# Optimization experiments

Hardware: AMD Instinct MI355X
Metric: run time of the kernel (lower is better)

The kernel has to match this reference:

```python
import jax, jax.numpy as jnp
import numpy as np

M = 4        # num_modalities
C = 128      # in_channels
NH = 4       # num_heads
HD = C // NH # head_dim = 32
OUT = 128    # out_channels
B, D, H, W = 1, 12, 12, 12
N = D * H * W
EPS = 1e-5
SCALE = float(np.sqrt(HD))


def setup_inputs() -> dict:
    key = jax.random.key(0)
    ks = jax.random.split(key, 12)
    inp = {}
    for i in range(M):
        inp[f"feat{i}"] = jax.random.normal(ks[i], (B, C, D, H, W), dtype=jnp.float32)
    s = 1.0 / np.sqrt(C)
    inp["Wq"] = jax.random.normal(ks[4], (M, C, C), dtype=jnp.float32) * s
    inp["Wk"] = jax.random.normal(ks[5], (M, C, C), dtype=jnp.float32) * s
    inp["Wv"] = jax.random.normal(ks[6], (M, C, C), dtype=jnp.float32) * s
    inp["Wout"] = jax.random.normal(ks[7], (OUT, C), dtype=jnp.float32) * s
    inp["bn_gamma"] = jnp.ones((OUT,), jnp.float32)
    inp["bn_beta"] = jnp.zeros((OUT,), jnp.float32)
    inp["bn_mean"] = jax.random.normal(ks[8], (OUT,), dtype=jnp.float32) * 0.1
    inp["bn_var"] = jax.random.uniform(ks[9], (OUT,), dtype=jnp.float32, minval=0.5, maxval=1.5)
    return inp


def _proj(Wm, feats):
    # per-modality 1x1 conv == matmul over channels: [M,C,C] x [M,B,C,N] -> [M,B,nh,N,hd]
    p = jnp.einsum('moc,mbcn->mbon', Wm, feats)
    return p.reshape(M, B, NH, HD, N).transpose(0, 1, 2, 4, 3)


def reference(feat0, feat1, feat2, feat3, Wq, Wk, Wv, Wout,
              bn_gamma, bn_beta, bn_mean, bn_var):
    feats = jnp.stack([feat0, feat1, feat2, feat3]).reshape(M, B, C, N)
    Q = _proj(Wq, feats)   # [M,B,nh,N,hd]
    K = _proj(Wk, feats)
    V = _proj(Wv, feats)
    # concat K/V over modalities along token axis -> [B,nh,M*N,hd]
    Kall = K.transpose(1, 2, 0, 3, 4).reshape(B, NH, M * N, HD)
    Vall = V.transpose(1, 2, 0, 3, 4).reshape(B, NH, M * N, HD)
    fused = jnp.zeros((B, NH, N, HD), jnp.float32)
    for i in range(M):  # small fixed loop over modalities
        attn = jnp.einsum('bhqd,bhkd->bhqk', Q[i], Kall) / SCALE  # [B,nh,N,M*N]
        attn = jax.nn.softmax(attn, axis=-1)  # dropout is identity at eval
        fused = fused + jnp.einsum('bhqk,bhkd->bhqd', attn, Vall)
    fused = fused.transpose(0, 1, 3, 2).reshape(B, C, N)
    # out_proj: 1x1 Conv3d -> BN (eval, running stats) -> ReLU
    y = jnp.einsum('oc,bcn->bon', Wout, fused)
    inv = bn_gamma / jnp.sqrt(bn_var + EPS)
    y = y * inv[None, :, None] + (bn_beta - bn_mean * inv)[None, :, None]
    return jax.nn.relu(y).reshape(B, OUT, D, H, W)
```

## Files before the change

kernel.cpp:

```cpp
#include <hip/hip_runtime.h>

#define MODS 4
#define CH   128
#define NHD  4
#define HDIM 32
#define NTOK 1728
#define NG   (NTOK/4)
#define NKEY (MODS*NTOK)
#define NT   27
#define QSC (0.17677669529663687f * 1.4426950408889634f)

#ifndef __has_builtin
#define __has_builtin(x) 0
#endif
#if __has_builtin(__builtin_amdgcn_exp2f)
#define EXP2(x) __builtin_amdgcn_exp2f(x)
#else
#define EXP2(x) __expf(0.69314718055994531f * (x))
#endif

typedef __bf16 bf16x8 __attribute__((ext_vector_type(8)));
typedef float  f32x16 __attribute__((ext_vector_type(16)));
typedef unsigned int u32x4 __attribute__((ext_vector_type(4)));

__device__ inline bf16x8 ldb8(const unsigned short* p) {
    return *reinterpret_cast<const bf16x8*>(p);
}
__device__ inline unsigned int pkbf(float a, float b) {
    unsigned short ua = __builtin_bit_cast(unsigned short, (__bf16)a);
    unsigned short ub = __builtin_bit_cast(unsigned short, (__bf16)b);
    return (unsigned int)ua | ((unsigned int)ub << 16);
}
__device__ inline void glds16(const unsigned short* g, unsigned short* l) {
    __builtin_amdgcn_global_load_lds(
        (const __attribute__((address_space(1))) unsigned int*)(g),
        (__attribute__((address_space(3))) unsigned int*)(l), 16, 0, 0);
}

__global__ __launch_bounds__(256) void proj_kernel(
    const float* __restrict__ f0, const float* __restrict__ f1,
    const float* __restrict__ f2, const float* __restrict__ f3,
    const float* __restrict__ Wq, const float* __restrict__ Wk,
    const float* __restrict__ Wv,
    unsigned short* __restrict__ Qb, unsigned short* __restrict__ Kb,
    unsigned short* __restrict__ V2)
{
    __shared__ __align__(16) float Wt[64][68];
    __shared__ __align__(16) float fs[64][68];

    const int tid = threadIdx.x;
    const int bid = blockIdx.x;
    const int tm  = bid / 54;
    const int rem = bid % 54;
    const int oh  = rem & 1;
    const int nt  = rem >> 1;
    const int t   = tm >> 2, m = tm & 3;
    const int nb  = nt * 64;

    const float* fsrc = (m == 0) ? f0 : (m == 1) ? f1 : (m == 2) ? f2 : f3;
    const float* W    = ((t == 0) ? Wq : (t == 1) ? Wk : Wv) + (size_t)m * CH * CH;

    const int o0 = (tid >> 4) * 4, nn0 = (tid & 15) * 4;
    float acc[4][4] = {};

    for (int ch = 0; ch < 2; ++ch) {
        if (ch) __syncthreads();
        {
            const int o = tid & 63, c4b = tid >> 6;
            #pragma unroll
            for (int j = 0; j < 4; ++j) {
                const int c4 = c4b + 4 * j;
                float4 wv = *reinterpret_cast<const float4*>(
                    W + (size_t)(oh * 64 + o) * CH + ch * 64 + c4 * 4);
                Wt[c4*4+0][o] = wv.x; Wt[c4*4+1][o] = wv.y;
                Wt[c4*4+2][o] = wv.z; Wt[c4*4+3][o] = wv.w;
            }
        }
        {
            const int nchunk = tid & 15, cb = tid >> 4;
            #pragma unroll
            for (int j = 0; j < 4; ++j) {
                const int c = cb + 16 * j;
                float4 v = *reinterpret_cast<const float4*>(
                    fsrc + (size_t)(ch * 64 + c) * NTOK + nb + nchunk * 4);
                *reinterpret_cast<float4*>(&fs[c][nchunk * 4]) = v;
            }
        }
        __syncthreads();
        #pragma unroll 4
        for (int c = 0; c < 64; ++c) {
            float4 wv = *reinterpret_cast<const float4*>(&Wt[c][o0]);
            float4 fv = *reinterpret_cast<const float4*>(&fs[c][nn0]);
            acc[0][0] = fmaf(wv.x, fv.x, acc[0][0]); acc[0][1] = fmaf(wv.x, fv.y, acc[0][1]);
            acc[0][2] = fmaf(wv.x, fv.z, acc[0][2]); acc[0][3] = fmaf(wv.x, fv.w, acc[0][3]);
            acc[1][0] = fmaf(wv.y, fv.x, acc[1][0]); acc[1][1] = fmaf(wv.y, fv.y, acc[1][1]);
            acc[1][2] = fmaf(wv.y, fv.z, acc[1][2]); acc[1][3] = fmaf(wv.y, fv.w, acc[1][3]);
            acc[2][0] = fmaf(wv.z, fv.x, acc[2][0]); acc[2][1] = fmaf(wv.z, fv.y, acc[2][1]);
            acc[2][2] = fmaf(wv.z, fv.z, acc[2][2]); acc[2][3] = fmaf(wv.z, fv.w, acc[2][3]);
            acc[3][0] = fmaf(wv.w, fv.x, acc[3][0]); acc[3][1] = fmaf(wv.w, fv.y, acc[3][1]);
            acc[3][2] = fmaf(wv.w, fv.z, acc[3][2]); acc[3][3] = fmaf(wv.w, fv.w, acc[3][3]);
        }
    }

    const int og0 = oh * 64 + o0;
    const int h = og0 >> 5, d0 = og0 & 31;
    const int ng = nb + nn0;
    if (t == 2) {
        const int off = ng & 15;
        const int ng2 = (ng & ~15) + ((off & 4) << 1) + ((off & 8) >> 1);
        #pragma unroll
        for (int i = 0; i < 4; ++i) {
            ushort4 pk;
            pk.x = __builtin_bit_cast(unsigned short, (__bf16)acc[i][0]);
            pk.y = __builtin_bit_cast(unsigned short, (__bf16)acc[i][1]);
            pk.z = __builtin_bit_cast(unsigned short, (__bf16)acc[i][2]);
            pk.w = __builtin_bit_cast(unsigned short, (__bf16)acc[i][3]);
            *reinterpret_cast<ushort4*>(V2 + (size_t)(h * HDIM + d0 + i) * NKEY + m * NTOK + ng2) = pk;
        }
    } else {
        const float sc = (t == 0) ? QSC : 1.0f;
        unsigned short* base = ((t == 0) ? Qb : Kb)
            + (((size_t)(m * NHD + h)) * NTOK + ng) * HDIM + d0;
        #pragma unroll
        for (int j = 0; j < 4; ++j) {
            unsigned short* row = base + (size_t)j * HDIM;
            *reinterpret_cast<unsigned int*>(row)     = pkbf(acc[0][j] * sc, acc[1][j] * sc);
            *reinterpret_cast<unsigned int*>(row + 2) = pkbf(acc[2][j] * sc, acc[3][j] * sc);
        }
    }
}

__global__ __launch_bounds__(256, 4) void attn_kernel(
    const unsigned short* __restrict__ Qb, const unsigned short* __restrict__ Kb,
    const unsigned short* __restrict__ V2,
    float* __restrict__ accT, float* __restrict__ sR)
{
    __shared__ __align__(16) unsigned short smAll[2][2][2][2048];

    const int tid  = threadIdx.x;
    const int lane = tid & 63;
    const int w    = tid >> 6;
    const int qslot = w & 1;
    const int ks    = w >> 1;
    const int l31  = lane & 31;
    const int hi   = lane >> 5;

    const int bid  = blockIdx.x;
    const int slot = bid & 7;
    const int h    = slot >> 1;
    const int ko   = slot & 1;
    const int qb   = bid >> 3;
    const int qtile = qb * 2 + qslot;
    const int qg0  = qtile * 32;
    const int im   = qg0 / NTOK;
    const int n0   = qg0 % NTOK;
    const int km   = ko * 2 + ks;

    const unsigned short* qp = Qb + (((size_t)(im * NHD + h)) * NTOK + n0 + l31) * HDIM + hi * 8;
    const bf16x8 qf0 = ldb8(qp);
    const bf16x8 qf1 = ldb8(qp + 16);

    const int rk0 = qslot * 32 + (lane >> 2);
    const int ck0 = (lane & 3) ^ ((rk0 >> 1) & 3);
    const unsigned short* gk0 = Kb + (((size_t)(km * NHD + h)) * NTOK + rk0) * HDIM + ck0 * 8;
    const int rk1 = rk0 + 16;
    const int ck1 = (lane & 3) ^ ((rk1 >> 1) & 3);
    const unsigned short* gk1 = Kb + (((size_t)(km * NHD + h)) * NTOK + rk1) * HDIM + ck1 * 8;
    const int dv0 = qslot * 16 + (lane >> 3);
    const int cv0 = (lane & 7) ^ (dv0 & 7);
    const unsigned short* gv0 = V2 + ((size_t)(h * HDIM + dv0)) * NKEY + km * NTOK + cv0 * 8;
    const int dv1 = dv0 + 8;
    const int cv1 = (lane & 7) ^ (dv1 & 7);
    const unsigned short* gv1 = V2 + ((size_t)(h * HDIM + dv1)) * NKEY + km * NTOK + cv1 * 8;

    const int f31 = (l31 >> 1) & 3;
    const int kA0 = l31 * 32 + ((hi ^ f31) << 3);
    const int kB0 = l31 * 32 + (((2 + hi) ^ f31) << 3);
    const int vbase = l31 * 64, x7 = l31 & 7;
    const int vo00 = vbase + (((0 + hi) ^ x7) << 3);
    const int vo01 = vbase + (((2 + hi) ^ x7) << 3);
    const int vo10 = vbase + (((4 + hi) ^ x7) << 3);
    const int vo11 = vbase + (((6 + hi) ^ x7) << 3);

    f32x16 z;
    #pragma unroll
    for (int r = 0; r < 16; ++r) z[r] = 0.f;
    f32x16 o_acc = z, s_acc = z;
    bf16x8 onesv;
    #pragma unroll
    for (int j = 0; j < 8; ++j) onesv[j] = (__bf16)1.0f;

    #define STAGE(bb) do {                                      \
        unsigned short* _k = &smAll[bb][ks][0][0];              \
        glds16(gk0, _k + qslot * 1024);                         \
        glds16(gk1, _k + qslot * 1024 + 512);                   \
        unsigned short* _v = &smAll[bb][ks][1][0];              \
        glds16(gv0, _v + qslot * 1024);                         \
        glds16(gv1, _v + qslot * 1024 + 512);                   \
        gk0 += 2048; gk1 += 2048; gv0 += 64; gv1 += 64;         \
    } while (0)

    STAGE(0);
    __syncthreads();

    int buf = 0;
    for (int t = 0; t < NT; ++t) {
        if (t + 1 < NT) STAGE(buf ^ 1);
        const unsigned short* Kl = &smAll[buf][ks][0][0];
        const unsigned short* Vl = &smAll[buf][ks][1][0];

        #pragma unroll
        for (int st = 0; st < 2; ++st) {
            bf16x8 k0 = ldb8(Kl + st * 1024 + kA0);
            bf16x8 k1 = ldb8(Kl + st * 1024 + kB0);
            f32x16 c = __builtin_amdgcn_mfma_f32_32x32x16_bf16(k0, qf0, z, 0, 0, 0);
            c = __builtin_amdgcn_mfma_f32_32x32x16_bf16(k1, qf1, c, 0, 0, 0);

            float e[16];
            #pragma unroll
            for (int r = 0; r < 16; ++r) e[r] = EXP2(c[r]);
            bf16x8 pa0, pa1;
            #pragma unroll
            for (int j = 0; j < 8; ++j) { pa0[j] = (__bf16)e[j]; pa1[j] = (__bf16)e[8 + j]; }

            bf16x8 v0 = ldb8(Vl + (st ? vo10 : vo00));
            bf16x8 v1 = ldb8(Vl + (st ? vo11 : vo01));

            o_acc = __builtin_amdgcn_mfma_f32_32x32x16_bf16(pa0, v0, o_acc, 0, 0, 0);
            o_acc = __builtin_amdgcn_mfma_f32_32x32x16_bf16(pa1, v1, o_acc, 0, 0, 0);
            s_acc = __builtin_amdgcn_mfma_f32_32x32x16_bf16(pa0, onesv, s_acc, 0, 0, 0);
            s_acc = __builtin_amdgcn_mfma_f32_32x32x16_bf16(pa1, onesv, s_acc, 0, 0, 0);
        }
        __syncthreads();
        buf ^= 1;
    }
    #undef STAGE

    float* accf = (float*)&smAll[0][0][0][0];
    if (ks == 1) {
        #pragma unroll
        for (int r = 0; r < 16; ++r) {
            const int qrow = (r & 3) + 8 * (r >> 2) + 4 * hi;
            accf[(qslot * 32 + qrow) * 33 + l31] = o_acc[r];
            if (l31 == 0) accf[(qslot * 32 + qrow) * 33 + 32] = s_acc[r];
        }
    }
    __syncthreads();
    if (ks == 0) {
        #pragma unroll
        for (int r = 0; r < 16; ++r) {
            const int qrow = (r & 3) + 8 * (r >> 2) + 4 * hi;
            accf[(qslot * 32 + qrow) * 33 + l31] += o_acc[r];
            if (l31 == 0) accf[(qslot * 32 + qrow) * 33 + 32] += s_acc[r];
        }
    }
    __syncthreads();
    {
        const int q  = tid & 63;
        const int dq = tid >> 6;
        #pragma unroll
        for (int j = 0; j < 8; ++j) {
            const int d = dq * 8 + j;
            accT[((size_t)((ko * 4 + h) * HDIM + d)) * NKEY + (size_t)qb * 64 + q]
                = accf[q * 33 + d];
        }
        if (tid < 64)
            sR[((size_t)(ko * 4 + h)) * NKEY + (size_t)qb * 64 + tid] = accf[tid * 33 + 32];
    }
}

__global__ __launch_bounds__(256) void norm_kernel(
    const float* __restrict__ accT, const float* __restrict__ sR,
    float* __restrict__ fused)
{
    const int idx = blockIdx.x * 256 + threadIdx.x;
    const int c = idx / NTOK;
    const int n = idx % NTOK;
    const int h = c >> 5;
    float acc = 0.f;
    #pragma unroll
    for (int imq = 0; imq < MODS; ++imq) {
        const size_t q = (size_t)imq * NTOK + n;
        const float s = sR[(size_t)h * NKEY + q] + sR[(size_t)(4 + h) * NKEY + q];
        const float a = accT[(size_t)c * NKEY + q] + accT[(size_t)(c + 128) * NKEY + q];
        acc = fmaf(a, 1.0f / s, acc);
    }
    fused[idx] = acc;
}

__global__ __launch_bounds__(256) void outproj_kernel(
    const float* __restrict__ fused, const float* __restrict__ Wout,
    const float* __restrict__ gamma, const float* __restrict__ beta,
    const float* __restrict__ mean,  const float* __restrict__ var,
    float* __restrict__ out)
{
    const int idx = blockIdx.x * 256 + threadIdx.x;
    const int n2 = idx % (NTOK / 2);
    const int o  = idx / (NTOK / 2);
    const float* W     = Wout + (size_t)o * CH;
    const float* fbase = fused + n2 * 2;
    float a0 = 0.f, a1 = 0.f;
    #pragma unroll 8
    for (int c = 0; c < CH; c += 4) {
        float4 w4 = *reinterpret_cast<const float4*>(W + c);
        float2 r0 = *reinterpret_cast<const float2*>(fbase + (size_t)(c + 0) * NTOK);
        float2 r1 = *reinterpret_cast<const float2*>(fbase + (size_t)(c + 1) * NTOK);
        float2 r2 = *reinterpret_cast<const float2*>(fbase + (size_t)(c + 2) * NTOK);
        float2 r3 = *reinterpret_cast<const float2*>(fbase + (size_t)(c + 3) * NTOK);
        a0 = fmaf(w4.x, r0.x, a0); a0 = fmaf(w4.y, r1.x, a0);
        a0 = fmaf(w4.z, r2.x, a0); a0 = fmaf(w4.w, r3.x, a0);
        a1 = fmaf(w4.x, r0.y, a1); a1 = fmaf(w4.y, r1.y, a1);
        a1 = fmaf(w4.z, r2.y, a1); a1 = fmaf(w4.w, r3.y, a1);
    }
    float inv = gamma[o] * rsqrtf(var[o] + 1e-5f);
    float sh  = fmaf(-mean[o], inv, beta[o]);
    float2 y;
    y.x = fmaxf(fmaf(a0, inv, sh), 0.f);
    y.y = fmaxf(fmaf(a1, inv, sh), 0.f);
    *reinterpret_cast<float2*>(out + (size_t)o * NTOK + n2 * 2) = y;
}

extern "C" void kernel_launch(void* const* d_in, const int* in_sizes, int n_in,
                              void* d_out, int out_size, void* d_ws, size_t ws_size,
                              hipStream_t stream)
{
    const float* f0    = (const float*)d_in[0];
    const float* f1    = (const float*)d_in[1];
    const float* f2    = (const float*)d_in[2];
    const float* f3    = (const float*)d_in[3];
    const float* Wq    = (const float*)d_in[4];
    const float* Wk    = (const float*)d_in[5];
    const float* Wv    = (const float*)d_in[6];
    const float* Wout  = (const float*)d_in[7];
    const float* gamma = (const float*)d_in[8];
    const float* beta  = (const float*)d_in[9];
    const float* mean  = (const float*)d_in[10];
    const float* var   = (const float*)d_in[11];
    float* out = (float*)d_out;

    const size_t QKV = (size_t)MODS * NHD * NTOK * HDIM;
    unsigned short* Qb = (unsigned short*)d_ws;
    unsigned short* Kb = Qb + QKV;
    unsigned short* V2 = Kb + QKV;
    float* accT  = (float*)(V2 + QKV);
    float* sR    = accT + (size_t)2 * NHD * HDIM * NKEY;
    float* fused = sR + (size_t)2 * NHD * NKEY;

    proj_kernel<<<648, 256, 0, stream>>>(f0, f1, f2, f3, Wq, Wk, Wv, Qb, Kb, V2);
    attn_kernel<<<864, 256, 0, stream>>>(Qb, Kb, V2, accT, sR);
    norm_kernel<<<(CH * NTOK) / 256, 256, 0, stream>>>(accT, sR, fused);
    outproj_kernel<<<(CH * NTOK / 2) / 256, 256, 0, stream>>>(
        fused, Wout, gamma, beta, mean, var, out);
}
```

Before: 79.38 us.

## Split attention key range into two segments and halve per-iteration key tile

Each attention block now covers half of a modality's keys (864 instead of 1728), so twice as many blocks are launched and four partial accumulators per head are written out and summed in the norm kernel. The per-iteration tile drops from 64 to 32 keys, which halves shared memory and allows a higher occupancy hint. This is meant to fill the GPU better and hide latency. In exchange it adds more partial-result traffic to global memory and more barriers per key processed.

```diff
diff --git a/kernel.cpp b/kernel.cpp
--- a/kernel.cpp
+++ b/kernel.cpp
@@ -21,7 +21,6 @@
 
 typedef __bf16 bf16x8 __attribute__((ext_vector_type(8)));
 typedef float  f32x16 __attribute__((ext_vector_type(16)));
-typedef unsigned int u32x4 __attribute__((ext_vector_type(4)));
 
 __device__ inline bf16x8 ldb8(const unsigned short* p) {
     return *reinterpret_cast<const bf16x8*>(p);
@@ -130,12 +129,12 @@
     }
 }
 
-__global__ __launch_bounds__(256, 4) void attn_kernel(
+__global__ __launch_bounds__(256, 8) void attn_kernel(
     const unsigned short* __restrict__ Qb, const unsigned short* __restrict__ Kb,
     const unsigned short* __restrict__ V2,
     float* __restrict__ accT, float* __restrict__ sR)
 {
-    __shared__ __align__(16) unsigned short smAll[2][2][2][2048];
+    __shared__ __align__(16) unsigned short smAll[2][2][2][1024];
 
     const int tid  = threadIdx.x;
     const int lane = tid & 63;
@@ -149,38 +148,34 @@
     const int slot = bid & 7;
     const int h    = slot >> 1;
     const int ko   = slot & 1;
-    const int qb   = bid >> 3;
+    const int rest = bid >> 3;
+    const int qb   = rest % 108;
+    const int kseg = rest / 108;
     const int qtile = qb * 2 + qslot;
     const int qg0  = qtile * 32;
     const int im   = qg0 / NTOK;
     const int n0   = qg0 % NTOK;
     const int km   = ko * 2 + ks;
+    const int p    = kseg * 2 + ko;
 
     const unsigned short* qp = Qb + (((size_t)(im * NHD + h)) * NTOK + n0 + l31) * HDIM + hi * 8;
     const bf16x8 qf0 = ldb8(qp);
     const bf16x8 qf1 = ldb8(qp + 16);
 
-    const int rk0 = qslot * 32 + (lane >> 2);
+    const int rk0 = qslot * 16 + (lane >> 2);
     const int ck0 = (lane & 3) ^ ((rk0 >> 1) & 3);
-    const unsigned short* gk0 = Kb + (((size_t)(km * NHD + h)) * NTOK + rk0) * HDIM + ck0 * 8;
-    const int rk1 = rk0 + 16;
-    const int ck1 = (lane & 3) ^ ((rk1 >> 1) & 3);
-    const unsigned short* gk1 = Kb + (((size_t)(km * NHD + h)) * NTOK + rk1) * HDIM + ck1 * 8;
-    const int dv0 = qslot * 16 + (lane >> 3);
-    const int cv0 = (lane & 7) ^ (dv0 & 7);
-    const unsigned short* gv0 = V2 + ((size_t)(h * HDIM + dv0)) * NKEY + km * NTOK + cv0 * 8;
-    const int dv1 = dv0 + 8;
-    const int cv1 = (lane & 7) ^ (dv1 & 7);
-    const unsigned short* gv1 = V2 + ((size_t)(h * HDIM + dv1)) * NKEY + km * NTOK + cv1 * 8;
-
-    const int f31 = (l31 >> 1) & 3;
-    const int kA0 = l31 * 32 + ((hi ^ f31) << 3);
-    const int kB0 = l31 * 32 + (((2 + hi) ^ f31) << 3);
-    const int vbase = l31 * 64, x7 = l31 & 7;
-    const int vo00 = vbase + (((0 + hi) ^ x7) << 3);
-    const int vo01 = vbase + (((2 + hi) ^ x7) << 3);
-    const int vo10 = vbase + (((4 + hi) ^ x7) << 3);
-    const int vo11 = vbase + (((6 + hi) ^ x7) << 3);
+    const unsigned short* gk0 = Kb
+        + (((size_t)(km * NHD + h)) * NTOK + kseg * 864 + rk0) * HDIM + ck0 * 8;
+    const int dv0 = qslot * 16 + (lane >> 2);
+    const int cv0 = (lane & 3) ^ (dv0 & 3);
+    const unsigned short* gv0 = V2
+        + ((size_t)(h * HDIM + dv0)) * NKEY + km * NTOK + kseg * 864 + cv0 * 8;
+
+    const int fK = (l31 >> 1) & 3, fV = l31 & 3;
+    const int kA0 = l31 * 32 + ((hi ^ fK) << 3);
+    const int kB0 = l31 * 32 + (((2 + hi) ^ fK) << 3);
+    const int vo0 = l31 * 32 + ((hi ^ fV) << 3);
+    const int vo1 = l31 * 32 + (((2 + hi) ^ fV) << 3);
 
     f32x16 z;
     #pragma unroll
@@ -191,13 +186,9 @@
     for (int j = 0; j < 8; ++j) onesv[j] = (__bf16)1.0f;
 
     #define STAGE(bb) do {                                      \
-        unsigned short* _k = &smAll[bb][ks][0][0];              \
-        glds16(gk0, _k + qslot * 1024);                         \
-        glds16(gk1, _k + qslot * 1024 + 512);                   \
-        unsigned short* _v = &smAll[bb][ks][1][0];              \
-        glds16(gv0, _v + qslot * 1024);                         \
-        glds16(gv1, _v + qslot * 1024 + 512);                   \
-        gk0 += 2048; gk1 += 2048; gv0 += 64; gv1 += 64;         \
+        glds16(gk0, &smAll[bb][ks][0][0] + qslot * 512);        \
+        glds16(gv0, &smAll[bb][ks][1][0] + qslot * 512);        \
+        gk0 += 1024; gv0 += 32;                                 \
     } while (0)
 
     STAGE(0);
@@ -209,28 +200,26 @@
         const unsigned short* Kl = &smAll[buf][ks][0][0];
         const unsigned short* Vl = &smAll[buf][ks][1][0];
 
-        #pragma unroll
-        for (int st = 0; st < 2; ++st) {
-            bf16x8 k0 = ldb8(Kl + st * 1024 + kA0);
-            bf16x8 k1 = ldb8(Kl + st * 1024 + kB0);
-            f32x16 c = __builtin_amdgcn_mfma_f32_32x32x16_bf16(k0, qf0, z, 0, 0, 0);
-            c = __builtin_amdgcn_mfma_f32_32x32x16_bf16(k1, qf1, c, 0, 0, 0);
-
-            float e[16];
-            #pragma unroll
-            for (int r = 0; r < 16; ++r) e[r] = EXP2(c[r]);
-            bf16x8 pa0, pa1;
-            #pragma unroll
-            for (int j = 0; j < 8; ++j) { pa0[j] = (__bf16)e[j]; pa1[j] = (__bf16)e[8 + j]; }
-
-            bf16x8 v0 = ldb8(Vl + (st ? vo10 : vo00));
-            bf16x8 v1 = ldb8(Vl + (st ? vo11 : vo01));
-
-            o_acc = __builtin_amdgcn_mfma_f32_32x32x16_bf16(pa0, v0, o_acc, 0, 0, 0);
-            o_acc = __builtin_amdgcn_mfma_f32_32x32x16_bf16(pa1, v1, o_acc, 0, 0, 0);
-            s_acc = __builtin_amdgcn_mfma_f32_32x32x16_bf16(pa0, onesv, s_acc, 0, 0, 0);
-            s_acc = __builtin_amdgcn_mfma_f32_32x32x16_bf16(pa1, onesv, s_acc, 0, 0, 0);
-        }
+        bf16x8 k0 = ldb8(Kl + kA0);
+        bf16x8 k1 = ldb8(Kl + kB0);
+        f32x16 c = __builtin_amdgcn_mfma_f32_32x32x16_bf16(k0, qf0, z, 0, 0, 0);
+        c = __builtin_amdgcn_mfma_f32_32x32x16_bf16(k1, qf1, c, 0, 0, 0);
+
+        float e[16];
+        #pragma unroll
+        for (int r = 0; r < 16; ++r) e[r] = EXP2(c[r]);
+        bf16x8 pa0, pa1;
+        #pragma unroll
+        for (int j = 0; j < 8; ++j) { pa0[j] = (__bf16)e[j]; pa1[j] = (__bf16)e[8 + j]; }
+
+        bf16x8 v0 = ldb8(Vl + vo0);
+        bf16x8 v1 = ldb8(Vl + vo1);
+
+        o_acc = __builtin_amdgcn_mfma_f32_32x32x16_bf16(pa0, v0, o_acc, 0, 0, 0);
+        o_acc = __builtin_amdgcn_mfma_f32_32x32x16_bf16(pa1, v1, o_acc, 0, 0, 0);
+        s_acc = __builtin_amdgcn_mfma_f32_32x32x16_bf16(pa0, onesv, s_acc, 0, 0, 0);
+        s_acc = __builtin_amdgcn_mfma_f32_32x32x16_bf16(pa1, onesv, s_acc, 0, 0, 0);
+
         __syncthreads();
         buf ^= 1;
     }
@@ -261,11 +250,11 @@
         #pragma unroll
         for (int j = 0; j < 8; ++j) {
             const int d = dq * 8 + j;
-            accT[((size_t)((ko * 4 + h) * HDIM + d)) * NKEY + (size_t)qb * 64 + q]
+            accT[((size_t)((p * 4 + h) * HDIM + d)) * NKEY + (size_t)qb * 64 + q]
                 = accf[q * 33 + d];
         }
         if (tid < 64)
-            sR[((size_t)(ko * 4 + h)) * NKEY + (size_t)qb * 64 + tid] = accf[tid * 33 + 32];
+            sR[((size_t)(p * 4 + h)) * NKEY + (size_t)qb * 64 + tid] = accf[tid * 33 + 32];
     }
 }
 
@@ -276,13 +265,17 @@
     const int idx = blockIdx.x * 256 + threadIdx.x;
     const int c = idx / NTOK;
     const int n = idx % NTOK;
-    const int h = c >> 5;
+    const int h = c >> 5, d = c & 31;
     float acc = 0.f;
     #pragma unroll
     for (int imq = 0; imq < MODS; ++imq) {
         const size_t q = (size_t)imq * NTOK + n;
-        const float s = sR[(size_t)h * NKEY + q] + sR[(size_t)(4 + h) * NKEY + q];
-        const float a = accT[(size_t)c * NKEY + q] + accT[(size_t)(c + 128) * NKEY + q];
+        float s = 0.f, a = 0.f;
+        #pragma unroll
+        for (int pp = 0; pp < 4; ++pp) {
+            s += sR[(size_t)(pp * 4 + h) * NKEY + q];
+            a += accT[((size_t)((pp * 4 + h) * HDIM + d)) * NKEY + q];
+        }
         acc = fmaf(a, 1.0f / s, acc);
     }
     fused[idx] = acc;
@@ -343,11 +336,11 @@
     unsigned short* Kb = Qb + QKV;
     unsigned short* V2 = Kb + QKV;
     float* accT  = (float*)(V2 + QKV);
-    float* sR    = accT + (size_t)2 * NHD * HDIM * NKEY;
-    float* fused = sR + (size_t)2 * NHD * NKEY;
+    float* sR    = accT + (size_t)4 * NHD * HDIM * NKEY;
+    float* fused = sR + (size_t)4 * NHD * NKEY;
 
     proj_kernel<<<648, 256, 0, stream>>>(f0, f1, f2, f3, Wq, Wk, Wv, Qb, Kb, V2);
-    attn_kernel<<<864, 256, 0, stream>>>(Qb, Kb, V2, accT, sR);
+    attn_kernel<<<1728, 256, 0, stream>>>(Qb, Kb, V2, accT, sR);
     norm_kernel<<<(CH * NTOK) / 256, 256, 0, stream>>>(accT, sR, fused);
     outproj_kernel<<<(CH * NTOK / 2) / 256, 256, 0, stream>>>(
         fused, Wout, gamma, beta, mean, var, out);
```

Result: slower. 136.0 us (+71.4%).
